# Kernel optimization log

Hardware: AMD Instinct MI355X
Metric: run time of the kernel (lower is better)

## Reference

```python
import jax, jax.numpy as jnp
import numpy as np

B, T, N, E, I, H = 8, 168, 425, 2048, 128, 256
F1, F2 = 10, 32  # GCN hidden dims


def gcn(x, src, dst, w, W, b):
    """PyG-style GCNConv on one graph: x [N,f_in], src/dst [E], w [E]."""
    n = x.shape[0]
    h = x @ W  # [N, f_out]
    sl = jnp.arange(n, dtype=src.dtype)  # self loops, weight 1
    s = jnp.concatenate([src, sl])
    d = jnp.concatenate([dst, sl])
    ww = jnp.concatenate([w, jnp.ones((n,), w.dtype)])
    deg = jax.ops.segment_sum(ww, d, num_segments=n)
    dinv = jnp.where(deg > 0, jax.lax.rsqrt(jnp.maximum(deg, 1e-12)), 0.0)
    norm = dinv[s] * ww * dinv[d]
    return jax.ops.segment_sum(norm[:, None] * h[s], d, num_segments=n) + b


# vectorize over (batch, time)
_gcn_bt = jax.vmap(jax.vmap(gcn, in_axes=(0, 0, 0, 0, None, None)),
                   in_axes=(0, 0, 0, 0, None, None))


def lstm(xs, h0, c0, Wih, Whh, bih, bhh):
    """Single-layer torch LSTM (gate order i,f,g,o). xs [B,T,I] -> [B,T,H]."""
    def step(carry, x):
        h, c = carry
        g = x @ Wih.T + h @ Whh.T + bih + bhh  # [B,4H]
        i, f, gg, o = jnp.split(g, 4, axis=-1)
        c = jax.nn.sigmoid(f) * c + jax.nn.sigmoid(i) * jnp.tanh(gg)
        h = jax.nn.sigmoid(o) * jnp.tanh(c)
        return (h, c), h
    _, ys = jax.lax.scan(step, (h0, c0), xs.transpose(1, 0, 2))
    return ys.transpose(1, 0, 2)


def setup_inputs() -> dict:
    key = jax.random.key(0)
    ks = jax.random.split(key, 40)
    def p(i, shape, s=0.05):
        return jax.random.normal(ks[i], shape, jnp.float32) * s
    return {
        "node_feat": jax.random.uniform(ks[0], (B, T, N), jnp.float32),
        "edge_src": jax.random.randint(ks[1], (B, T, E), 0, N, jnp.int32),
        "edge_dst": jax.random.randint(ks[2], (B, T, E), 0, N, jnp.int32),
        "edge_weight": jax.random.uniform(ks[3], (B, T, E), jnp.float32),
        "infect": p(4, (B, T, 25), 1.0),
        "temp": p(5, (B, T, 13), 1.0),
        "h0": p(6, (1, B, H), 1.0),
        "c0": p(7, (1, B, H), 1.0),
        "Wg1": p(8, (1, F1)), "bg1": p(9, (F1,)),
        "Wg2": p(10, (F1, F2)), "bg2": p(11, (F2,)),
        "Wgfc": p(12, (N * F2, I)), "bgfc": p(13, (I,)),
        "Wi1": p(14, (25, 128)), "bi1": p(15, (128,)),
        "Wi2": p(16, (128, 128)), "bi2": p(17, (128,)),
        "Wi3": p(18, (128, 64)), "bi3": p(19, (64,)),
        "Wi4": p(20, (64, I)), "bi4": p(21, (I,)),
        "Wt1": p(22, (13, 64)), "bt1": p(23, (64,)),
        "Wt2": p(24, (64, I)), "bt2": p(25, (I,)),
        "Wcat": p(26, (3 * I, I)), "bcat": p(27, (I,)),
        "Wih": p(28, (4 * H, I)), "Whh": p(29, (4 * H, H)),
        "bih": p(30, (4 * H,)), "bhh": p(31, (4 * H,)),
        "Wfc": p(32, (H, 2 * N)), "bfc": p(33, (2 * N,)),
    }


def reference(node_feat, edge_src, edge_dst, edge_weight, infect, temp, h0, c0,
              Wg1, bg1, Wg2, bg2, Wgfc, bgfc,
              Wi1, bi1, Wi2, bi2, Wi3, bi3, Wi4, bi4,
              Wt1, bt1, Wt2, bt2, Wcat, bcat,
              Wih, Whh, bih, bhh, Wfc, bfc):
    r = jax.nn.relu
    # two-layer GCN per (batch, timestep) graph (deep_graph path)
    x1 = r(_gcn_bt(node_feat[..., None], edge_src, edge_dst, edge_weight, Wg1, bg1))
    x2 = r(_gcn_bt(x1, edge_src, edge_dst, edge_weight, Wg2, bg2))
    g = r(x2.reshape(B, T, N * F2) @ Wgfc + bgfc)  # graph branch [B,T,I]
    inf = r(infect @ Wi1 + bi1)
    inf = r(inf @ Wi2 + bi2)
    inf = r(inf @ Wi3 + bi3)
    inf = r(inf @ Wi4 + bi4)  # infect branch [B,T,I]
    tp = r(temp @ Wt1 + bt1)
    tp = r(tp @ Wt2 + bt2)  # temp branch [B,T,I]
    li = r(jnp.concatenate([g, inf, tp], axis=-1) @ Wcat + bcat)  # concat_fc path
    ys = r(lstm(li, h0[0], c0[0], Wih, Whh, bih, bhh))  # [B,T,H]
    out = r(ys[:, -1] @ Wfc + bfc)  # [B, 2N]
    # original splits by flattening the whole [B,2N] tensor
    flat = out.reshape(-1)
    user_pred = flat[: N * B].reshape(B, N)
    infect_pred = flat[N * B:].reshape(B, N)
    return user_pred, infect_pred
```

## Files before the change

### kernel.cpp

```cpp
#include <hip/hip_runtime.h>
#include <hip/hip_bf16.h>

#define BB 8
#define TT 168
#define NN 425
#define EE 2048
#define II 128
#define HH 256
#define F1 10
#define F2 32
#define BT (BB*TT)
#define K2 (NN*F2)
#define N2 (2*NN)

#define BREG_PW 46
#define BLDS_PW 18
#define BREG_N (8*BREG_PW*64)
#define BLDS_N (8*BLDS_PW*64)

#define FR_TOTAL 444

typedef _Float16 h2 __attribute__((ext_vector_type(2)));
typedef _Float16 h8 __attribute__((ext_vector_type(8)));
typedef short bf16x8 __attribute__((ext_vector_type(8)));
typedef float f32x4 __attribute__((ext_vector_type(4)));

__device__ __forceinline__ float relu_(float x){ return fmaxf(x, 0.f); }
__device__ __forceinline__ float sigmoid_(float x){ return 1.f/(1.f + expf(-x)); }

#define MFMA16(ACC, AV, BV) \
    ACC = __builtin_amdgcn_mfma_f32_16x16x32_f16((AV), (BV), (ACC), 0, 0, 0)

__device__ __forceinline__ void ds_pk_add(h2* p, h2 v){
    unsigned a = (unsigned)(uintptr_t)p;
    asm volatile("ds_pk_add_f16 %0, %1" :: "v"(a), "v"(v) : "memory");
}

__device__ __forceinline__ h8 actld(const char* act, int K, int lane, int kc){
    int row = lane & 15;
    unsigned off = ((unsigned)(row*K + kc*32 + ((lane>>4)<<3))*2) ^ (unsigned)((row&7)<<4);
    return *(const h8*)(act + off);
}
__device__ __forceinline__ void actst(char* act, int K, int row, int col, _Float16 v){
    unsigned off = ((unsigned)(row*K + col)*2) ^ (unsigned)((row&7)<<4);
    *(_Float16*)(act + off) = v;
}

__global__ __launch_bounds__(256) void gcn_kernel(
    const float* __restrict__ nf, const int* __restrict__ esrc,
    const int* __restrict__ edst, const float* __restrict__ ew,
    const float* __restrict__ Wg1, const float* __restrict__ bg1,
    const float* __restrict__ Wg2, const float* __restrict__ bg2,
    __hip_bfloat16* __restrict__ x2g)
{
    __shared__ float xs[NN];
    __shared__ float dinv[NN];
    __shared__ float agg1[NN];
    __shared__ float nrm[EE];
    __shared__ __align__(16) float x1p[NN*12];
    __shared__ __align__(16) h2 agg2h[NN*8];
    __shared__ float wg1s[F1], bg1s[F1], wg2s[F1*F2], bg2s[F2];

    const int bt = blockIdx.x, tid = threadIdx.x;
    const long eb = (long)bt * EE;

    for (int v = tid; v < NN; v += 256) {
        xs[v] = nf[(long)bt*NN + v];
        dinv[v] = 1.0f;
        agg1[v] = 0.f;
    }
    for (int i = tid; i < NN*8; i += 256) agg2h[i] = (h2){(_Float16)0.f, (_Float16)0.f};
    if (tid < F1) { wg1s[tid] = Wg1[tid]; bg1s[tid] = bg1[tid]; }
    if (tid < F2) bg2s[tid] = bg2[tid];
    for (int i = tid; i < F1*F2; i += 256) wg2s[i] = Wg2[i];
    __syncthreads();

    for (int e = tid; e < EE; e += 256)
        atomicAdd(&dinv[edst[eb+e]], ew[eb+e]);
    __syncthreads();
    for (int v = tid; v < NN; v += 256) {
        float dg = dinv[v];
        dinv[v] = dg > 0.f ? 1.0f / sqrtf(fmaxf(dg, 1e-12f)) : 0.f;
    }
    __syncthreads();

    for (int e = tid; e < EE; e += 256) {
        int s = esrc[eb+e], d = edst[eb+e];
        float nm = dinv[s] * ew[eb+e] * dinv[d];
        nrm[e] = nm;
        atomicAdd(&agg1[d], nm * xs[s]);
    }
    __syncthreads();
    for (int v = tid; v < NN; v += 256) agg1[v] += dinv[v]*dinv[v]*xs[v];
    __syncthreads();
    for (int i = tid; i < NN*12; i += 256) {
        int v = i / 12, f = i - v*12;
        x1p[i] = (f < F1) ? relu_(agg1[v]*wg1s[f] + bg1s[f]) : 0.f;
    }
    __syncthreads();

    for (int e = tid; e < EE; e += 256) {
        int s = esrc[eb+e], d = edst[eb+e];
        float nm = nrm[e];
        float4 a0 = *(const float4*)&x1p[s*12];
        float4 a1 = *(const float4*)&x1p[s*12+4];
        float2 a2 = *(const float2*)&x1p[s*12+8];
        h2 p0; p0[0] = (_Float16)(nm*a0.x); p0[1] = (_Float16)(nm*a0.y);
        h2 p1; p1[0] = (_Float16)(nm*a0.z); p1[1] = (_Float16)(nm*a0.w);
        h2 p2; p2[0] = (_Float16)(nm*a1.x); p2[1] = (_Float16)(nm*a1.y);
        h2 p3; p3[0] = (_Float16)(nm*a1.z); p3[1] = (_Float16)(nm*a1.w);
        h2 p4; p4[0] = (_Float16)(nm*a2.x); p4[1] = (_Float16)(nm*a2.y);
        ds_pk_add(&agg2h[d*8+0], p0);
        ds_pk_add(&agg2h[d*8+1], p1);
        ds_pk_add(&agg2h[d*8+2], p2);
        ds_pk_add(&agg2h[d*8+3], p3);
        ds_pk_add(&agg2h[d*8+4], p4);
    }
    __syncthreads();

    {
        const int k = tid & 31;
        float wk[F1];
        #pragma unroll
        for (int f = 0; f < F1; ++f) wk[f] = wg2s[f*F2 + k];
        for (int i = tid; i < NN*F2; i += 256) {
            int v = i >> 5;
            float dv2 = dinv[v]*dinv[v];
            h8 r8 = *(const h8*)&agg2h[v*8];
            h2 r2 = agg2h[v*8+4];
            float4 a0 = *(const float4*)&x1p[v*12];
            float4 a1 = *(const float4*)&x1p[v*12+4];
            float2 a2 = *(const float2*)&x1p[v*12+8];
            float af[10];
            af[0]=(float)r8[0]+dv2*a0.x; af[1]=(float)r8[1]+dv2*a0.y;
            af[2]=(float)r8[2]+dv2*a0.z; af[3]=(float)r8[3]+dv2*a0.w;
            af[4]=(float)r8[4]+dv2*a1.x; af[5]=(float)r8[5]+dv2*a1.y;
            af[6]=(float)r8[6]+dv2*a1.z; af[7]=(float)r8[7]+dv2*a1.w;
            af[8]=(float)r2[0]+dv2*a2.x; af[9]=(float)r2[1]+dv2*a2.y;
            float o = bg2s[k];
            #pragma unroll
            for (int f = 0; f < F1; ++f) o += af[f]*wk[f];
            x2g[(long)bt*K2 + i] = __float2bfloat16(relu_(o));
        }
    }
}

__global__ __launch_bounds__(256) void packT_kernel(
    const float* __restrict__ W, __hip_bfloat16* __restrict__ out)
{
    __shared__ float tile[64][129];
    const int k0 = blockIdx.x * 64, tid = threadIdx.x;
    for (int i = tid; i < 64*128; i += 256) {
        int r = i >> 7, j = i & 127;
        tile[r][j] = (k0 + r < K2) ? W[(size_t)(k0+r)*II + j] : 0.f;
    }
    __syncthreads();
    for (int i = tid; i < 64*128; i += 256) {
        int j = i >> 6, r = i & 63;
        if (k0 + r < K2) out[(size_t)j*K2 + k0 + r] = __float2bfloat16(tile[r][j]);
    }
}

#define GBM 64
#define GBK 64
#define GCH 8
#define GST 27
__global__ __launch_bounds__(256) void gemm_kernel(
    const __hip_bfloat16* __restrict__ A, const __hip_bfloat16* __restrict__ Bt,
    float* __restrict__ C)
{
    __shared__ __align__(16) char As[2][GBM*GBK*2];
    __shared__ __align__(16) char Bs[2][II*GBK*2];
    const int tid = threadIdx.x;
    const int row0 = blockIdx.x * GBM;
    const int kbeg = blockIdx.y * (GST*GBK);
    const int wave = tid >> 6, lane = tid & 63;
    const int wm = wave >> 1, wn = wave & 1;
    const int l16 = lane & 15, lk = lane >> 4;
    const short* Aa = (const short*)A;
    const short* Bb = (const short*)Bt;

    const int ar = tid >> 2, ac = tid & 3;
    const int bc = tid >> 1, bh = (tid & 1) * 4;

    f32x4 acc[2][4];
    #pragma unroll
    for (int m = 0; m < 2; ++m)
        #pragma unroll
        for (int n = 0; n < 4; ++n) acc[m][n] = (f32x4){0.f,0.f,0.f,0.f};

    {
        #pragma unroll
        for (int j = 0; j < 2; ++j) {
            bf16x8 va = {0,0,0,0,0,0,0,0};
            int k = kbeg + ac*16 + j*8;
            if (k < K2) va = *(const bf16x8*)(Aa + (size_t)(row0+ar)*K2 + k);
            *(bf16x8*)(&As[0][0] + ((ar*128 + (ac*2+j)*16) ^ ((ar&7)<<4))) = va;
        }
        #pragma unroll
        for (int j = 0; j < 4; ++j) {
            bf16x8 vb = {0,0,0,0,0,0,0,0};
            int k = kbeg + (bh+j)*8;
            if (k < K2) vb = *(const bf16x8*)(Bb + (size_t)bc*K2 + k);
            *(bf16x8*)(&Bs[0][0] + ((bc*128 + (bh+j)*16) ^ ((bc&7)<<4))) = vb;
        }
    }
    __syncthreads();

    for (int s = 0; s < GST; ++s) {
        const int d = s & 1;
        bf16x8 pa[2], pb[4];
        #pragma unroll
        for (int j = 0; j < 2; ++j) pa[j] = (bf16x8){0,0,0,0,0,0,0,0};
        #pragma unroll
        for (int j = 0; j < 4; ++j) pb[j] = (bf16x8){0,0,0,0,0,0,0,0};
        if (s + 1 < GST) {
            int k0n = kbeg + (s+1)*GBK;
            #pragma unroll
            for (int j = 0; j < 2; ++j) {
                int k = k0n + ac*16 + j*8;
                if (k < K2) pa[j] = *(const bf16x8*)(Aa + (size_t)(row0+ar)*K2 + k);
            }
            #pragma unroll
            for (int j = 0; j < 4; ++j) {
                int k = k0n + (bh+j)*8;
                if (k < K2) pb[j] = *(const bf16x8*)(Bb + (size_t)bc*K2 + k);
            }
        }
        #pragma unroll
        for (int s2 = 0; s2 < 2; ++s2) {
            bf16x8 af[2], bf[4];
            #pragma unroll
            for (int m = 0; m < 2; ++m) {
                int row = wm*32 + m*16 + l16;
                af[m] = *(const bf16x8*)(&As[d][0] + ((row*128 + s2*64 + lk*16) ^ ((row&7)<<4)));
            }
            #pragma unroll
            for (int n = 0; n < 4; ++n) {
                int col = wn*64 + n*16 + l16;
                bf[n] = *(const bf16x8*)(&Bs[d][0] + ((col*128 + s2*64 + lk*16) ^ ((col&7)<<4)));
            }
            #pragma unroll
            for (int m = 0; m < 2; ++m)
                #pragma unroll
                for (int n = 0; n < 4; ++n)
                    acc[m][n] = __builtin_amdgcn_mfma_f32_16x16x32_bf16(af[m], bf[n], acc[m][n], 0, 0, 0);
        }
        if (s + 1 < GST) {
            #pragma unroll
            for (int j = 0; j < 2; ++j)
                *(bf16x8*)(&As[d^1][0] + ((ar*128 + (ac*2+j)*16) ^ ((ar&7)<<4))) = pa[j];
            #pragma unroll
            for (int j = 0; j < 4; ++j)
                *(bf16x8*)(&Bs[d^1][0] + ((bc*128 + (bh+j)*16) ^ ((bc&7)<<4))) = pb[j];
        }
        __syncthreads();
    }

    #pragma unroll
    for (int m = 0; m < 2; ++m)
        #pragma unroll
        for (int n = 0; n < 4; ++n)
            #pragma unroll
            for (int q = 0; q < 4; ++q)
                atomicAdd(&C[(size_t)(row0 + wm*32 + m*16 + lk*4 + q)*II + wn*64 + n*16 + l16],
                          acc[m][n][q]);
}

__global__ __launch_bounds__(64) void pack_frags_kernel(
    const float* __restrict__ Wi1, const float* __restrict__ Wi2,
    const float* __restrict__ Wi3, const float* __restrict__ Wi4,
    const float* __restrict__ Wt1, const float* __restrict__ Wt2,
    const float* __restrict__ Wcat, const float* __restrict__ Wih,
    h8* __restrict__ out)
{
    int f = blockIdx.x, l = threadIdx.x;
    const float* S; int sn, sk, K, KC, base;
    if      (f < 8)   { S=Wi1;  sn=1;   sk=128; K=25;  KC=1;  base=0;  }
    else if (f < 40)  { S=Wi2;  sn=1;   sk=128; K=128; KC=4;  base=8;  }
    else if (f < 56)  { S=Wi3;  sn=1;   sk=64;  K=128; KC=4;  base=40; }
    else if (f < 72)  { S=Wi4;  sn=1;   sk=128; K=64;  KC=2;  base=56; }
    else if (f < 76)  { S=Wt1;  sn=1;   sk=64;  K=13;  KC=1;  base=72; }
    else if (f < 92)  { S=Wt2;  sn=1;   sk=128; K=64;  KC=2;  base=76; }
    else if (f < 188) { S=Wcat; sn=1;   sk=128; K=384; KC=12; base=92; }
    else              { S=Wih;  sn=128; sk=1;   K=128; KC=4;  base=188;}
    int loc = f - base, nt = loc / KC, kc = loc % KC;
    int n = nt*16 + (l & 15);
    int k0 = kc*32 + ((l >> 4) << 3);
    h8 v;
    #pragma unroll
    for (int e = 0; e < 8; ++e) {
        int k = k0 + e;
        v[e] = (_Float16)((k < K) ? S[(size_t)n*sn + (size_t)k*sk] : 0.f);
    }
    out[(size_t)f*64 + l] = v;
}

__global__ __launch_bounds__(256) void blx_kernel(
    const float* __restrict__ infect, const float* __restrict__ temp,
    const float* __restrict__ g_pre, const float* __restrict__ bgfc,
    const float* __restrict__ bi1, const float* __restrict__ bi2,
    const float* __restrict__ bi3, const float* __restrict__ bi4,
    const float* __restrict__ bt1, const float* __restrict__ bt2,
    const float* __restrict__ bcat, const float* __restrict__ bih,
    const float* __restrict__ bhh, const h8* __restrict__ frags,
    float* __restrict__ xg)
{
    __shared__ __align__(16) char CAT[16*384*2];
    __shared__ __align__(16) char S0[16*128*2];
    __shared__ __align__(16) char S1[16*128*2];
    __shared__ __align__(16) char LIb[16*128*2];
    __shared__ __align__(16) char XIN[16*32*2];
    __shared__ __align__(16) char XTt[16*32*2];
    __shared__ __align__(16) char XT1[16*64*2];

    const int tid = threadIdx.x, lane = tid & 63, w = tid >> 6;
    const int r0 = blockIdx.x * 16;
    const int c16 = lane & 15;
    const int rq = (lane >> 4) * 4;

    for (int i = tid; i < 16*32; i += 256) {
        int r = i >> 5, c = i & 31;
        actst(XIN, 32, r, c, (_Float16)((c < 25) ? infect[(size_t)(r0+r)*25 + c] : 0.f));
        actst(XTt, 32, r, c, (_Float16)((c < 13) ? temp[(size_t)(r0+r)*13 + c] : 0.f));
    }
    for (int i = tid; i < 16*128; i += 256) {
        int r = i >> 7, u = i & 127;
        actst(CAT, 384, r, u, (_Float16)relu_(g_pre[(size_t)(r0+r)*128 + u] + bgfc[u]));
    }
    __syncthreads();

    {
        h8 a = actld(XIN, 32, lane, 0);
        #pragma unroll
        for (int nt = w; nt < 8; nt += 4) {
            f32x4 acc = (f32x4){0.f,0.f,0.f,0.f};
            MFMA16(acc, a, frags[(size_t)(0 + nt)*64 + lane]);
            float bv = bi1[nt*16 + c16];
            #pragma unroll
            for (int q = 0; q < 4; ++q)
                actst(S0, 128, rq + q, nt*16 + c16, (_Float16)relu_(acc[q] + bv));
        }
        h8 at = actld(XTt, 32, lane, 0);
        {
            int nt = w;
            f32x4 acc = (f32x4){0.f,0.f,0.f,0.f};
            MFMA16(acc, at, frags[(size_t)(72 + nt)*64 + lane]);
            float bv = bt1[nt*16 + c16];
            #pragma unroll
            for (int q = 0; q < 4; ++q)
                actst(XT1, 64, rq + q, nt*16 + c16, (_Float16)relu_(acc[q] + bv));
        }
    }
    __syncthreads();

    {
        h8 a[4];
        #pragma unroll
        for (int kc = 0; kc < 4; ++kc) a[kc] = actld(S0, 128, lane, kc);
        #pragma unroll
        for (int nt = w; nt < 8; nt += 4) {
            f32x4 acc = (f32x4){0.f,0.f,0.f,0.f};
            #pragma unroll
            for (int kc = 0; kc < 4; ++kc)
                MFMA16(acc, a[kc], frags[(size_t)(8 + nt*4 + kc)*64 + lane]);
            float bv = bi2[nt*16 + c16];
            #pragma unroll
            for (int q = 0; q < 4; ++q)
                actst(S1, 128, rq + q, nt*16 + c16, (_Float16)relu_(acc[q] + bv));
        }
        h8 a2[2];
        #pragma unroll
        for (int kc = 0; kc < 2; ++kc) a2[kc] = actld(XT1, 64, lane, kc);
        #pragma unroll
        for (int nt = w; nt < 8; nt += 4) {
            f32x4 acc = (f32x4){0.f,0.f,0.f,0.f};
            #pragma unroll
            for (int kc = 0; kc < 2; ++kc)
                MFMA16(acc, a2[kc], frags[(size_t)(76 + nt*2 + kc)*64 + lane]);
            float bv = bt2[nt*16 + c16];
            #pragma unroll
            for (int q = 0; q < 4; ++q)
                actst(CAT, 384, rq + q, 256 + nt*16 + c16, (_Float16)relu_(acc[q] + bv));
        }
    }
    __syncthreads();

    {
        h8 a[4];
        #pragma unroll
        for (int kc = 0; kc < 4; ++kc) a[kc] = actld(S1, 128, lane, kc);
        int nt = w;
        f32x4 acc = (f32x4){0.f,0.f,0.f,0.f};
        #pragma unroll
        for (int kc = 0; kc < 4; ++kc)
            MFMA16(acc, a[kc], frags[(size_t)(40 + nt*4 + kc)*64 + lane]);
        float bv = bi3[nt*16 + c16];
        #pragma unroll
        for (int q = 0; q < 4; ++q)
            actst(XT1, 64, rq + q, nt*16 + c16, (_Float16)relu_(acc[q] + bv));
    }
    __syncthreads();

    {
        h8 a[2];
        #pragma unroll
        for (int kc = 0; kc < 2; ++kc) a[kc] = actld(XT1, 64, lane, kc);
        #pragma unroll
        for (int nt = w; nt < 8; nt += 4) {
            f32x4 acc = (f32x4){0.f,0.f,0.f,0.f};
            #pragma unroll
            for (int kc = 0; kc < 2; ++kc)
                MFMA16(acc, a[kc], frags[(size_t)(56 + nt*2 + kc)*64 + lane]);
            float bv = bi4[nt*16 + c16];
            #pragma unroll
            for (int q = 0; q < 4; ++q)
                actst(CAT, 384, rq + q, 128 + nt*16 + c16, (_Float16)relu_(acc[q] + bv));
        }
    }
    __syncthreads();

    {
        h8 a[12];
        #pragma unroll
        for (int kc = 0; kc < 12; ++kc) a[kc] = actld(CAT, 384, lane, kc);
        #pragma unroll
        for (int nt = w; nt < 8; nt += 4) {
            f32x4 acc = (f32x4){0.f,0.f,0.f,0.f};
            #pragma unroll
            for (int kc = 0; kc < 12; ++kc)
                MFMA16(acc, a[kc], frags[(size_t)(92 + nt*12 + kc)*64 + lane]);
            float bv = bcat[nt*16 + c16];
            #pragma unroll
            for (int q = 0; q < 4; ++q)
                actst(LIb, 128, rq + q, nt*16 + c16, (_Float16)relu_(acc[q] + bv));
        }
    }
    __syncthreads();

    {
        h8 a[4];
        #pragma unroll
        for (int kc = 0; kc < 4; ++kc) a[kc] = actld(LIb, 128, lane, kc);
        for (int nt = w; nt < 64; nt += 4) {
            f32x4 acc = (f32x4){0.f,0.f,0.f,0.f};
            #pragma unroll
            for (int kc = 0; kc < 4; ++kc)
                MFMA16(acc, a[kc], frags[(size_t)(188 + nt*4 + kc)*64 + lane]);
            int n = nt*16 + c16;
            float bv = bih[n] + bhh[n];
            #pragma unroll
            for (int q = 0; q < 4; ++q)
                xg[(size_t)(r0 + rq + q)*1024 + n] = acc[q] + bv;
        }
    }
}

__global__ __launch_bounds__(256) void pack_whh_kernel(
    const float* __restrict__ Whh, h8* __restrict__ bregp,
    h8* __restrict__ bldsp)
{
    int i = blockIdx.x*256 + threadIdx.x;
    int w, j, kc, lane;
    bool isreg = (i < BREG_N);
    if (isreg) {
        w = i / (BREG_PW*64); int r = i % (BREG_PW*64);
        int fidx = r >> 6; lane = r & 63;
        j  = (fidx < 42) ? fidx / 6 : 7;
        kc = (fidx < 42) ? fidx % 6 : fidx - 42;
    } else {
        int L = i - BREG_N;
        if (L >= BLDS_N) return;
        w = L / (BLDS_PW*64); int r = L % (BLDS_PW*64);
        int fidx = r >> 6; lane = r & 63;
        j  = (fidx < 14) ? (fidx >> 1) : 7;
        kc = (fidx < 14) ? 6 + (fidx & 1) : 4 + (fidx - 14);
    }
    int row = 128*w + 16*j + (lane & 15);
    int col = 32*kc + 8*(lane >> 4);
    h8 v;
    #pragma unroll
    for (int e = 0; e < 8; ++e) v[e] = (_Float16)Whh[(long)row*HH + col + e];
    if (isreg) bregp[i] = v; else bldsp[i - BREG_N] = v;
}

__attribute__((amdgpu_waves_per_eu(2, 2)))
__global__ __launch_bounds__(512) void lstm_kernel(
    const float* __restrict__ xg, const h8* __restrict__ bregp,
    const h8* __restrict__ bldsp, const float* __restrict__ h0,
    const float* __restrict__ c0, float* __restrict__ hbuf)
{
    const int u = threadIdx.x;
    const int lane = u & 63;
    const int w = u >> 6;
    const int b = blockIdx.x;

    __shared__ __align__(16) h8 wlds[BLDS_N];
    __shared__ float gbuf[1024];
    __shared__ __align__(16) _Float16 harr[2][HH];

    for (int i = u; i < BLDS_N; i += 512) wlds[i] = bldsp[i];

    h8 bfr[BREG_PW];
    {
        const h8* bp = bregp + (size_t)(w*BREG_PW)*64 + lane;
        #pragma unroll
        for (int m = 0; m < BREG_PW; ++m) bfr[m] = bp[(size_t)m*64];
    }

    float c = 0.f, h_last = 0.f;
    if (u < 256) { c = c0[b*HH + u]; harr[0][u] = (_Float16)h0[b*HH + u]; }
    __syncthreads();

    const float* xgb = xg + (size_t)b*TT*1024;
    const char* wbase = (const char*)wlds + w*(BLDS_PW*1024);
    const char* hbase = (const char*)harr;
    const int q16 = (lane >> 4) << 4;

    #pragma unroll 1
    for (int t = 0; t < TT; ++t) {
        const int cb = t & 1;
        float x0 = 0.f, x1 = 0.f, x2 = 0.f, x3 = 0.f;
        if (u < 256) {
            x0 = xgb[t*1024 + u];        x1 = xgb[t*1024 + 256 + u];
            x2 = xgb[t*1024 + 512 + u];  x3 = xgb[t*1024 + 768 + u];
        }
        h8 a[8];
        #pragma unroll
        for (int kc = 0; kc < 8; ++kc)
            a[kc] = *(const h8*)(hbase + cb*512 + kc*64 + q16);

        #pragma unroll
        for (int j = 0; j < 8; ++j) {
            f32x4 acc = (f32x4){0.f, 0.f, 0.f, 0.f};
            #pragma unroll
            for (int kc = 0; kc < 8; ++kc) {
                h8 bv;
                if ((j < 7) ? (kc < 6) : (kc < 4)) {
                    bv = bfr[(j < 7) ? (j*6 + kc) : (42 + kc)];
                } else {
                    unsigned off = (unsigned)(((j < 7) ? (j*2 + kc - 6)
                                                       : (14 + kc - 4))*1024 + lane*16);
                    asm volatile("" : "+v"(off));
                    bv = *(const h8*)(wbase + off);
                }
                acc = __builtin_amdgcn_mfma_f32_16x16x32_f16(a[kc], bv, acc, 0, 0, 0);
            }
            if (lane < 16) gbuf[w*128 + j*16 + lane] = acc[0];
        }
        __syncthreads();
        if (u < 256) {
            float gi = gbuf[u]       + x0;
            float gf = gbuf[256 + u] + x1;
            float gg = gbuf[512 + u] + x2;
            float go = gbuf[768 + u] + x3;
            c = sigmoid_(gf)*c + sigmoid_(gi)*tanhf(gg);
            float h = sigmoid_(go)*tanhf(c);
            harr[cb ^ 1][u] = (_Float16)h;
            h_last = h;
        }
        __syncthreads();
    }
    if (u < 256) hbuf[b*HH + u] = h_last;
}

__global__ __launch_bounds__(256) void final_fc_kernel(
    const float* __restrict__ hbuf, const float* __restrict__ Wfc,
    const float* __restrict__ bfc, float* __restrict__ out)
{
    int idx = blockIdx.x*256 + threadIdx.x;
    if (idx >= BB*N2) return;
    int b = idx / N2, j = idx - b*N2;
    const float* h = hbuf + b*HH;
    float o = bfc[j];
    for (int k = 0; k < HH; ++k) o += fmaxf(h[k], 0.f) * Wfc[(long)k*N2 + j];
    out[idx] = relu_(o);
}

extern "C" void kernel_launch(void* const* d_in, const int* in_sizes, int n_in,
                              void* d_out, int out_size, void* d_ws, size_t ws_size,
                              hipStream_t stream) {
    const float* nf     = (const float*)d_in[0];
    const int*   esrc   = (const int*)d_in[1];
    const int*   edst   = (const int*)d_in[2];
    const float* ew     = (const float*)d_in[3];
    const float* infect = (const float*)d_in[4];
    const float* temp   = (const float*)d_in[5];
    const float* h0     = (const float*)d_in[6];
    const float* c0     = (const float*)d_in[7];
    const float* Wg1    = (const float*)d_in[8];
    const float* bg1    = (const float*)d_in[9];
    const float* Wg2    = (const float*)d_in[10];
    const float* bg2    = (const float*)d_in[11];
    const float* Wgfc   = (const float*)d_in[12];
    const float* bgfc   = (const float*)d_in[13];
    const float* Wi1    = (const float*)d_in[14];
    const float* bi1    = (const float*)d_in[15];
    const float* Wi2    = (const float*)d_in[16];
    const float* bi2    = (const float*)d_in[17];
    const float* Wi3    = (const float*)d_in[18];
    const float* bi3    = (const float*)d_in[19];
    const float* Wi4    = (const float*)d_in[20];
    const float* bi4    = (const float*)d_in[21];
    const float* Wt1    = (const float*)d_in[22];
    const float* bt1    = (const float*)d_in[23];
    const float* Wt2    = (const float*)d_in[24];
    const float* bt2    = (const float*)d_in[25];
    const float* Wcat   = (const float*)d_in[26];
    const float* bcat   = (const float*)d_in[27];
    const float* Wih    = (const float*)d_in[28];
    const float* Whh    = (const float*)d_in[29];
    const float* bih    = (const float*)d_in[30];
    const float* bhh    = (const float*)d_in[31];
    const float* Wfc    = (const float*)d_in[32];
    const float* bfc    = (const float*)d_in[33];

    char* ws = (char*)d_ws;
    size_t off = 0;
    __hip_bfloat16* x2g = (__hip_bfloat16*)(ws + off); off += (size_t)BT*K2*2;
    __hip_bfloat16* WgfcT = (__hip_bfloat16*)(ws + off); off += (size_t)II*K2*2;
    float* g_pre = (float*)(ws + off); off += (size_t)BT*II*4;
    float* xg    = (float*)(ws + off); off += (size_t)BT*1024*4;
    float* hbuf  = (float*)(ws + off); off += (size_t)BB*HH*4;
    h8* bregp = (h8*)(ws + off); off += (size_t)BREG_N*16;
    h8* bldsp = (h8*)(ws + off); off += (size_t)BLDS_N*16;
    h8* frags = (h8*)(ws + off); off += (size_t)FR_TOTAL*64*16;

    hipMemsetAsync(g_pre, 0, (size_t)BT*II*4, stream);

    pack_whh_kernel<<<128, 256, 0, stream>>>(Whh, bregp, bldsp);
    pack_frags_kernel<<<FR_TOTAL, 64, 0, stream>>>(Wi1, Wi2, Wi3, Wi4, Wt1, Wt2,
                                                   Wcat, Wih, frags);
    packT_kernel<<<(K2 + 63)/64, 256, 0, stream>>>(Wgfc, WgfcT);
    gcn_kernel<<<BT, 256, 0, stream>>>(nf, esrc, edst, ew, Wg1, bg1, Wg2, bg2, x2g);
    gemm_kernel<<<dim3(BT/GBM, GCH), 256, 0, stream>>>(x2g, WgfcT, g_pre);
    blx_kernel<<<BT/16, 256, 0, stream>>>(infect, temp, g_pre, bgfc,
                                          bi1, bi2, bi3, bi4, bt1, bt2,
                                          bcat, bih, bhh, frags, xg);
    lstm_kernel<<<BB, 512, 0, stream>>>(xg, bregp, bldsp, h0, c0, hbuf);
    final_fc_kernel<<<(BB*N2 + 255)/256, 256, 0, stream>>>(hbuf, Wfc, bfc, (float*)d_out);
}
```

Measured before the change: 602.9 us.

## Process two batch rows per LSTM block and interleave gate inputs for float4 loads

```diff
diff --git a/kernel.cpp b/kernel.cpp
--- a/kernel.cpp
+++ b/kernel.cpp
@@ -17,6 +17,7 @@
 #define BLDS_PW 18
 #define BREG_N (8*BREG_PW*64)
 #define BLDS_N (8*BLDS_PW*64)
+#define LB 2
 
 #define FR_TOTAL 444
 
@@ -304,7 +305,7 @@
     const float* __restrict__ bt1, const float* __restrict__ bt2,
     const float* __restrict__ bcat, const float* __restrict__ bih,
     const float* __restrict__ bhh, const h8* __restrict__ frags,
-    float* __restrict__ xg)
+    float* __restrict__ xg4)
 {
     __shared__ __align__(16) char CAT[16*384*2];
     __shared__ __align__(16) char S0[16*128*2];
@@ -448,10 +449,11 @@
             for (int kc = 0; kc < 4; ++kc)
                 MFMA16(acc, a[kc], frags[(size_t)(188 + nt*4 + kc)*64 + lane]);
             int n = nt*16 + c16;
+            int uu = n & 255, gg = n >> 8;
             float bv = bih[n] + bhh[n];
             #pragma unroll
             for (int q = 0; q < 4; ++q)
-                xg[(size_t)(r0 + rq + q)*1024 + n] = acc[q] + bv;
+                xg4[(size_t)(r0 + rq + q)*1024 + uu*4 + gg] = acc[q] + bv;
         }
     }
 }
@@ -486,18 +488,20 @@
 
 __attribute__((amdgpu_waves_per_eu(2, 2)))
 __global__ __launch_bounds__(512) void lstm_kernel(
-    const float* __restrict__ xg, const h8* __restrict__ bregp,
+    const float* __restrict__ xg4, const h8* __restrict__ bregp,
     const h8* __restrict__ bldsp, const float* __restrict__ h0,
     const float* __restrict__ c0, float* __restrict__ hbuf)
 {
     const int u = threadIdx.x;
     const int lane = u & 63;
     const int w = u >> 6;
-    const int b = blockIdx.x;
+    const int b0 = blockIdx.x * LB;
+    const int bb = u >> 8, un = u & 255;
+    const int Bg = b0 + bb;
 
     __shared__ __align__(16) h8 wlds[BLDS_N];
-    __shared__ float gbuf[1024];
-    __shared__ __align__(16) _Float16 harr[2][HH];
+    __shared__ float gbuf[LB*1024];
+    __shared__ __align__(16) char hbytes[2][LB*512];
 
     for (int i = u; i < BLDS_N; i += 512) wlds[i] = bldsp[i];
 
@@ -508,27 +512,25 @@
         for (int m = 0; m < BREG_PW; ++m) bfr[m] = bp[(size_t)m*64];
     }
 
-    float c = 0.f, h_last = 0.f;
-    if (u < 256) { c = c0[b*HH + u]; harr[0][u] = (_Float16)h0[b*HH + u]; }
-    __syncthreads();
-
-    const float* xgb = xg + (size_t)b*TT*1024;
+    float c = c0[Bg*HH + un];
+    float h_last = 0.f;
+    *(_Float16*)(&hbytes[0][0] + ((bb*512 + un*2) ^ (bb<<4))) = (_Float16)h0[Bg*HH + un];
+    __syncthreads();
+
     const char* wbase = (const char*)wlds + w*(BLDS_PW*1024);
-    const char* hbase = (const char*)harr;
-    const int q16 = (lane >> 4) << 4;
+    const int br = lane & 1;
+    const unsigned abase = (unsigned)((br*512 + ((lane>>4)<<3)*2) ^ (br<<4));
+    const float4* xp = (const float4*)xg4;
 
     #pragma unroll 1
     for (int t = 0; t < TT; ++t) {
         const int cb = t & 1;
-        float x0 = 0.f, x1 = 0.f, x2 = 0.f, x3 = 0.f;
-        if (u < 256) {
-            x0 = xgb[t*1024 + u];        x1 = xgb[t*1024 + 256 + u];
-            x2 = xgb[t*1024 + 512 + u];  x3 = xgb[t*1024 + 768 + u];
-        }
+        float4 xv = xp[((size_t)Bg*TT + t)*256 + un];
+
         h8 a[8];
         #pragma unroll
         for (int kc = 0; kc < 8; ++kc)
-            a[kc] = *(const h8*)(hbase + cb*512 + kc*64 + q16);
+            a[kc] = *(const h8*)(&hbytes[cb][0] + (abase ^ (unsigned)(kc*64)));
 
         #pragma unroll
         for (int j = 0; j < 8; ++j) {
@@ -546,22 +548,27 @@
                 }
                 acc = __builtin_amdgcn_mfma_f32_16x16x32_f16(a[kc], bv, acc, 0, 0, 0);
             }
-            if (lane < 16) gbuf[w*128 + j*16 + lane] = acc[0];
+            if (lane < 16) {
+                int n = 128*w + j*16 + lane;
+                gbuf[n]        = acc[0];
+                gbuf[1024 + n] = acc[1];
+            }
         }
         __syncthreads();
-        if (u < 256) {
-            float gi = gbuf[u]       + x0;
-            float gf = gbuf[256 + u] + x1;
-            float gg = gbuf[512 + u] + x2;
-            float go = gbuf[768 + u] + x3;
+
+        {
+            float gi = gbuf[bb*1024 + un]       + xv.x;
+            float gf = gbuf[bb*1024 + 256 + un] + xv.y;
+            float gg = gbuf[bb*1024 + 512 + un] + xv.z;
+            float go = gbuf[bb*1024 + 768 + un] + xv.w;
             c = sigmoid_(gf)*c + sigmoid_(gi)*tanhf(gg);
             float h = sigmoid_(go)*tanhf(c);
-            harr[cb ^ 1][u] = (_Float16)h;
+            *(_Float16*)(&hbytes[cb^1][0] + ((bb*512 + un*2) ^ (bb<<4))) = (_Float16)h;
             h_last = h;
         }
         __syncthreads();
     }
-    if (u < 256) hbuf[b*HH + u] = h_last;
+    hbuf[Bg*HH + un] = h_last;
 }
 
 __global__ __launch_bounds__(256) void final_fc_kernel(
@@ -620,7 +627,7 @@
     __hip_bfloat16* x2g = (__hip_bfloat16*)(ws + off); off += (size_t)BT*K2*2;
     __hip_bfloat16* WgfcT = (__hip_bfloat16*)(ws + off); off += (size_t)II*K2*2;
     float* g_pre = (float*)(ws + off); off += (size_t)BT*II*4;
-    float* xg    = (float*)(ws + off); off += (size_t)BT*1024*4;
+    float* xg4   = (float*)(ws + off); off += (size_t)BT*1024*4;
     float* hbuf  = (float*)(ws + off); off += (size_t)BB*HH*4;
     h8* bregp = (h8*)(ws + off); off += (size_t)BREG_N*16;
     h8* bldsp = (h8*)(ws + off); off += (size_t)BLDS_N*16;
@@ -636,7 +643,7 @@
     gemm_kernel<<<dim3(BT/GBM, GCH), 256, 0, stream>>>(x2g, WgfcT, g_pre);
     blx_kernel<<<BT/16, 256, 0, stream>>>(infect, temp, g_pre, bgfc,
                                           bi1, bi2, bi3, bi4, bt1, bt2,
-                                          bcat, bih, bhh, frags, xg);
-    lstm_kernel<<<BB, 512, 0, stream>>>(xg, bregp, bldsp, h0, c0, hbuf);
+                                          bcat, bih, bhh, frags, xg4);
+    lstm_kernel<<<BB/LB, 512, 0, stream>>>(xg4, bregp, bldsp, h0, c0, hbuf);
     final_fc_kernel<<<(BB*N2 + 255)/256, 256, 0, stream>>>(hbuf, Wfc, bfc, (float*)d_out);
 }
```

New measurement: 572.4 us. -5.1%, faster.
